# Kernel tuning notes

Measured on AMD Instinct MI355X. Metric: run time of the kernel, lower is better.

The kernel has to match this reference:

```python
import jax, jax.numpy as jnp
import numpy as np

LN2 = 0.6931471805599453

def ssp(t):
    # PhysNet shifted softplus
    return jax.nn.softplus(t) - LN2

N, F, K, E, NRES = 50000, 128, 64, 800000, 3

def setup_inputs() -> dict:
    key = jax.random.key(0)
    ks = jax.random.split(key, 16)
    d = {}
    d['x'] = jax.random.normal(ks[0], (N, F), dtype=jnp.float32)
    d['edge_index'] = jax.random.randint(ks[1], (2, E), 0, N, dtype=jnp.int64)
    d['edge_attr'] = jax.random.uniform(ks[2], (E, K), dtype=jnp.float32)
    s = 1.0 / np.sqrt(F)
    d['W_same'] = jax.random.normal(ks[3], (F, F), dtype=jnp.float32) * s
    d['b_same'] = jnp.zeros((F,), jnp.float32)
    d['W_diff'] = jax.random.normal(ks[4], (F, F), dtype=jnp.float32) * s
    d['b_diff'] = jnp.zeros((F,), jnp.float32)
    # G initialized to zero in the original; use small random so gradients flow
    d['W_G'] = jax.random.normal(ks[5], (F, K), dtype=jnp.float32) * 0.01
    d['res_W1'] = jax.random.normal(ks[6], (NRES, F, F), dtype=jnp.float32) * s
    d['res_b1'] = jnp.zeros((NRES, F), jnp.float32)
    d['res_W2'] = jax.random.normal(ks[7], (NRES, F, F), dtype=jnp.float32) * s
    d['res_b2'] = jnp.zeros((NRES, F), jnp.float32)
    d['W_last'] = jax.random.normal(ks[8], (F, F), dtype=jnp.float32) * s
    d['b_last'] = jnp.zeros((F,), jnp.float32)
    d['u'] = jnp.ones((1, F), jnp.float32)
    return d

def reference(x, edge_index, edge_attr, W_same, b_same, W_diff, b_diff, W_G,
              res_W1, res_b1, res_W2, res_b2, W_last, b_last, u):
    src, dst = edge_index[0], edge_index[1]  # flow='source_to_target': x_j = x[src], aggr at dst
    xa = ssp(x)                                           # activation(x) before propagate
    # message: act(lin_for_diff(x_j)) -- linear+act commute with gather, compute per-node
    h = ssp(xa @ W_diff.T + b_diff)                       # [N, F]
    gate = edge_attr @ W_G.T                              # [E, F]  G(edge_attr)
    msg = h[src] * gate                                   # [E, F]
    aggr = jax.ops.segment_sum(msg, dst, num_segments=x.shape[0])  # add-aggregate
    # update: act(lin_for_same(x)) + aggr_out
    msged_x = ssp(xa @ W_same.T + b_same) + aggr          # [N, F]
    # residual interaction layers: t + lin2(act(lin1(act(t))))
    t = msged_x
    for i in range(res_W1.shape[0]):
        h1 = ssp(ssp(t) @ res_W1[i].T + res_b1[i])
        t = t + (h1 @ res_W2[i].T + res_b2[i])
    v = ssp(t) @ W_last.T + b_last
    return (v + x * u, msged_x)
```

## Files before the change

kernel.cpp:

```cpp
#include <hip/hip_runtime.h>
#include <hip/hip_bf16.h>

#define LN2F 0.69314718055994530942f

typedef short bf16x8 __attribute__((ext_vector_type(8)));
typedef float f32x4  __attribute__((ext_vector_type(4)));

__device__ __forceinline__ float ssp_f(float t){
  return fmaxf(t, 0.0f) + __logf(1.0f + __expf(-fabsf(t))) - LN2F;
}
__device__ __forceinline__ unsigned short f2bf_u(float f){
  __hip_bfloat16 b = __float2bfloat16(f);
  return *reinterpret_cast<unsigned short*>(&b);
}
__device__ __forceinline__ float bf2f(unsigned short u){
  __hip_bfloat16 b = *reinterpret_cast<__hip_bfloat16*>(&u);
  return __bfloat162float(b);
}

__device__ __forceinline__ int load_idx(const void* ei, int is32, size_t pos){
  return is32 ? ((const int*)ei)[pos] : (int)(((const long long*)ei)[pos]);
}

struct WPtrs { const float* w[16]; };

__global__ __launch_bounds__(256) void setup_prep_kernel(
    const unsigned* __restrict__ ei, int* __restrict__ flag,
    int* __restrict__ count, int N, int nzb,
    WPtrs p, int nw, unsigned short* __restrict__ wfrag,
    const float* __restrict__ WG, unsigned short* __restrict__ wgfrag){
  const int m = blockIdx.x;
  if (m < nzb){
    int i = m * 256 + threadIdx.x;
    if (i < N) count[i] = 0;
    if (m == 0){
      __shared__ int cnt;
      if (threadIdx.x == 0) cnt = 0;
      __syncthreads();
      int nz = 0;
      for (int k = threadIdx.x; k < 1024; k += 256)
        nz += (ei[2*k + 1] != 0u) ? 1 : 0;
      atomicAdd(&cnt, nz);
      __syncthreads();
      if (threadIdx.x == 0) *flag = (cnt > 64) ? 1 : 0;
    }
  } else if (m < nzb + nw){
    const int w = m - nzb;
    const float* __restrict__ W = p.w[w];
    unsigned short* __restrict__ out = wfrag + (size_t)w * 16384;
    for (int q = threadIdx.x; q < 16384; q += 256){
      int i = q & 7, lane = (q >> 3) & 63, kt = (q >> 9) & 3, ct = q >> 11;
      int row = ct*16 + (lane & 15);
      int k   = kt*32 + (lane >> 4)*8 + i;
      out[q] = f2bf_u(W[row*128 + k]);
    }
  } else {
    const int b = m - nzb - nw;
    for (int qq = threadIdx.x; qq < 2048; qq += 256){
      int q = b*2048 + qq;
      int i = q & 7, lane = (q >> 3) & 63, kt = (q >> 9) & 1, nt = q >> 10;
      int f = nt*16 + (lane & 15);
      int k = kt*32 + (lane >> 4)*8 + i;
      wgfrag[q] = f2bf_u(WG[(size_t)f*64 + k]);
    }
  }
}

__global__ void hist_kernel(const void* __restrict__ ei, const int* __restrict__ flag,
                            int* __restrict__ count, int E){
  const int is32 = *flag;
  for (long long e = (long long)blockIdx.x * 256 + threadIdx.x; e < E;
       e += (long long)gridDim.x * 256){
    int d = load_idx(ei, is32, (size_t)((long long)E + e));
    atomicAdd(&count[d], 1);
  }
}

__global__ __launch_bounds__(256) void scan1_kernel(const int* __restrict__ count,
                                                    int* __restrict__ bsum, int N){
  __shared__ int red[256];
  const int t = threadIdx.x;
  int i0 = blockIdx.x * 2048 + t * 8;
  int s = 0;
  #pragma unroll
  for (int r = 0; r < 8; ++r){ int i = i0 + r; s += (i < N) ? count[i] : 0; }
  red[t] = s;
  __syncthreads();
  for (int off = 128; off > 0; off >>= 1){
    if (t < off) red[t] += red[t + off];
    __syncthreads();
  }
  if (t == 0) bsum[blockIdx.x] = red[0];
}

__global__ void scan2_kernel(int* __restrict__ bsum, int* __restrict__ offs, int nb, int N){
  if (threadIdx.x == 0 && blockIdx.x == 0){
    int run = 0;
    for (int b = 0; b < nb; ++b){ int v = bsum[b]; bsum[b] = run; run += v; }
    offs[N] = run;
  }
}

__global__ __launch_bounds__(256) void scan3_kernel(const int* __restrict__ count,
                                                    const int* __restrict__ bsum,
                                                    int* __restrict__ offs,
                                                    int* __restrict__ cur, int N){
  __shared__ int red[256];
  const int t = threadIdx.x;
  int i0 = blockIdx.x * 2048 + t * 8;
  int v[8];
  int s = 0;
  #pragma unroll
  for (int r = 0; r < 8; ++r){ int i = i0 + r; v[r] = (i < N) ? count[i] : 0; s += v[r]; }
  red[t] = s;
  __syncthreads();
  #pragma unroll
  for (int off = 1; off < 256; off <<= 1){
    int tv = (t >= off) ? red[t - off] : 0;
    __syncthreads();
    red[t] += tv;
    __syncthreads();
  }
  int run = red[t] - s + bsum[blockIdx.x];
  #pragma unroll
  for (int r = 0; r < 8; ++r){
    int i = i0 + r;
    if (i < N){ offs[i] = run; cur[i] = run; }
    run += v[r];
  }
}

__global__ void fill_kernel(const void* __restrict__ ei, const int* __restrict__ flag,
                            int* __restrict__ cur, int2* __restrict__ se, int E){
  const int is32 = *flag;
  for (long long e = (long long)blockIdx.x * 256 + threadIdx.x; e < E;
       e += (long long)gridDim.x * 256){
    int s = load_idx(ei, is32, (size_t)e);
    int d = load_idx(ei, is32, (size_t)((long long)E + e));
    int slot = atomicAdd(&cur[d], 1);
    se[slot] = make_int2((int)e, s);
  }
}

__device__ __forceinline__ void mfma_gemm128s(const unsigned short* __restrict__ A_s,
                                              const unsigned short* __restrict__ Bf,
                                              int rbase, int lane, f32x4 acc[8]){
  #pragma unroll
  for (int ct = 0; ct < 8; ++ct) acc[ct] = (f32x4){0.f, 0.f, 0.f, 0.f};
  const int r  = rbase + (lane & 15);
  const int kg = lane >> 4;
  const int sw = (r & 7) << 3;
  #pragma unroll
  for (int kt = 0; kt < 4; ++kt){
    bf16x8 a = *(const bf16x8*)&A_s[r*128 + ((kt*32 + kg*8) ^ sw)];
    #pragma unroll
    for (int ct = 0; ct < 8; ++ct){
      bf16x8 b = *(const bf16x8*)&Bf[(size_t)((ct*4 + kt)*64 + lane)*8];
      acc[ct] = __builtin_amdgcn_mfma_f32_16x16x32_bf16(a, b, acc[ct], 0, 0, 0);
    }
  }
}

__device__ __forceinline__ void stage_bf512(unsigned short* __restrict__ Bf,
                                            const unsigned short* __restrict__ src, int t){
  #pragma unroll
  for (int it = 0; it < 4; ++it){
    int off = (it*512 + t) * 8;
    *(uint4*)&Bf[off] = *(const uint4*)&src[off];
  }
}

__global__ __launch_bounds__(512) void node_dual_kernel(
    const float* __restrict__ x, const unsigned short* __restrict__ wfrag,
    const float* __restrict__ bsame, const float* __restrict__ bdiff,
    unsigned short* __restrict__ hbf, float* __restrict__ msged, int N){
  __shared__ __align__(16) unsigned short A_s[128*128];
  __shared__ __align__(16) unsigned short Bf[16384];
  const int t = threadIdx.x, wv = t >> 6, lane = t & 63;
  const int kg = lane >> 4, c = lane & 15;
  const int row0 = blockIdx.x * 128;
  for (int q = t; q < 2048; q += 512){
    int row = q >> 4, c0 = (q & 15) * 8;
    float4 va = make_float4(0.f,0.f,0.f,0.f), vb = va;
    if (row0 + row < N){
      va = *(const float4*)&x[(size_t)(row0 + row)*128 + c0];
      vb = *(const float4*)&x[(size_t)(row0 + row)*128 + c0 + 4];
    }
    uint4 w;
    w.x = f2bf_u(ssp_f(va.x)) | ((unsigned)f2bf_u(ssp_f(va.y)) << 16);
    w.y = f2bf_u(ssp_f(va.z)) | ((unsigned)f2bf_u(ssp_f(va.w)) << 16);
    w.z = f2bf_u(ssp_f(vb.x)) | ((unsigned)f2bf_u(ssp_f(vb.y)) << 16);
    w.w = f2bf_u(ssp_f(vb.z)) | ((unsigned)f2bf_u(ssp_f(vb.w)) << 16);
    *(uint4*)&A_s[row*128 + (c0 ^ ((row & 7) << 3))] = w;
  }
  stage_bf512(Bf, wfrag, t);
  __syncthreads();
  f32x4 acc[8];
  mfma_gemm128s(A_s, Bf, wv*16, lane, acc);
  #pragma unroll
  for (int ct = 0; ct < 8; ++ct){
    int col = ct*16 + c;
    float bv = bsame[col];
    #pragma unroll
    for (int q = 0; q < 4; ++q){
      int gr = row0 + wv*16 + kg*4 + q;
      if (gr < N) msged[(size_t)gr*128 + col] = ssp_f(acc[ct][q] + bv);
    }
  }
  __syncthreads();
  stage_bf512(Bf, wfrag + 16384, t);
  __syncthreads();
  mfma_gemm128s(A_s, Bf, wv*16, lane, acc);
  #pragma unroll
  for (int ct = 0; ct < 8; ++ct){
    int col = ct*16 + c;
    float bv = bdiff[col];
    #pragma unroll
    for (int q = 0; q < 4; ++q){
      int gr = row0 + wv*16 + kg*4 + q;
      if (gr < N) hbf[(size_t)gr*128 + col] = f2bf_u(ssp_f(acc[ct][q] + bv));
    }
  }
}

__global__ __launch_bounds__(256) void edge_mfma_kernel(
    const float* __restrict__ ea, const unsigned short* __restrict__ wgfrag,
    const unsigned short* __restrict__ h, const int2* __restrict__ se,
    const int* __restrict__ offs, float* __restrict__ msged, int N, int E, int KW){
  __shared__ float gate_s[4][16][132];
  __shared__ unsigned short h_s[4][16][136];
  const int t = threadIdx.x, wv = t >> 6, lane = t & 63;
  const int kg = lane >> 4, c = lane & 15;
  const int widx = blockIdx.x * 4 + wv;
  if (widx >= KW) return;
  long long tt0 = (long long)widx * E / KW;
  long long tt1 = (long long)(widx + 1) * E / KW;
  int lo = 0, hi = N;
  while (lo < hi){ int mid = (lo + hi) >> 1; if ((long long)offs[mid] < tt0) lo = mid + 1; else hi = mid; }
  const int d_lo = lo;
  hi = N;
  while (lo < hi){ int mid = (lo + hi) >> 1; if ((long long)offs[mid] < tt1) lo = mid + 1; else hi = mid; }
  const int d_hi = lo;
  if (d_lo >= d_hi) return;
  const int s_beg = offs[d_lo], s_end = offs[d_hi];
  if (s_beg >= s_end) return;

  bf16x8 aw[8][2];
  #pragma unroll
  for (int nt = 0; nt < 8; ++nt)
    #pragma unroll
    for (int kt = 0; kt < 2; ++kt)
      aw[nt][kt] = *(const bf16x8*)&wgfrag[(size_t)(((nt*2+kt)*64)+lane)*8];

  int d_cur = d_lo;
  int no0 = offs[d_cur + 1];
  while (no0 == s_beg && d_cur + 1 < d_hi){ ++d_cur; no0 = offs[d_cur + 1]; }
  int no1 = (d_cur + 2 <= d_hi) ? offs[d_cur + 2] : 0x7FFFFFFF;

  float sum0 = 0.f, sum1 = 0.f;
  int p = s_beg;
  int nb = min(16, s_end - p);
  int2 s2 = se[p + min(c, nb - 1)];
  while (p < s_end){
    const int pn = p + 16;
    int2 s2n = s2;
    if (pn < s_end){
      int nbn = min(16, s_end - pn);
      s2n = se[pn + min(c, nbn - 1)];
    }
    const float* __restrict__ ra = &ea[(size_t)s2.x * 64 + kg*8];
    float4 e00 = *(const float4*)&ra[0];
    float4 e01 = *(const float4*)&ra[4];
    float4 e10 = *(const float4*)&ra[32];
    float4 e11 = *(const float4*)&ra[36];

    uint4 hreg[4];
    #pragma unroll
    for (int it = 0; it < 4; ++it){
      int j = it*64 + lane;
      int row = j >> 4, seg = j & 15;
      int sr = __shfl(s2.y, row, 16);
      hreg[it] = *(const uint4*)&h[(size_t)sr*128 + seg*8];
    }
    #pragma unroll
    for (int it = 0; it < 4; ++it){
      int j = it*64 + lane;
      int row = j >> 4, seg = j & 15;
      *(uint4*)&h_s[wv][row][seg*8] = hreg[it];
    }

    bf16x8 be0, be1;
    unsigned short* b0p = (unsigned short*)&be0;
    unsigned short* b1p = (unsigned short*)&be1;
    b0p[0]=f2bf_u(e00.x); b0p[1]=f2bf_u(e00.y); b0p[2]=f2bf_u(e00.z); b0p[3]=f2bf_u(e00.w);
    b0p[4]=f2bf_u(e01.x); b0p[5]=f2bf_u(e01.y); b0p[6]=f2bf_u(e01.z); b0p[7]=f2bf_u(e01.w);
    b1p[0]=f2bf_u(e10.x); b1p[1]=f2bf_u(e10.y); b1p[2]=f2bf_u(e10.z); b1p[3]=f2bf_u(e10.w);
    b1p[4]=f2bf_u(e11.x); b1p[5]=f2bf_u(e11.y); b1p[6]=f2bf_u(e11.z); b1p[7]=f2bf_u(e11.w);

    #pragma unroll
    for (int nt = 0; nt < 8; ++nt){
      f32x4 acc = (f32x4){0.f,0.f,0.f,0.f};
      acc = __builtin_amdgcn_mfma_f32_16x16x32_bf16(aw[nt][0], be0, acc, 0, 0, 0);
      acc = __builtin_amdgcn_mfma_f32_16x16x32_bf16(aw[nt][1], be1, acc, 0, 0, 0);
      *(f32x4*)&gate_s[wv][c][nt*16 + kg*4] = acc;
    }

    asm volatile("s_waitcnt lgkmcnt(0)" ::: "memory");

    const int nbc = min(16, s_end - p);
    #pragma unroll
    for (int i = 0; i < 16; ++i){
      if (i < nbc){
        float g0 = gate_s[wv][i][lane];
        float g1 = gate_s[wv][i][lane + 64];
        float h0 = bf2f(h_s[wv][i][lane]);
        float h1 = bf2f(h_s[wv][i][lane + 64]);
        sum0 = __builtin_fmaf(g0, h0, sum0);
        sum1 = __builtin_fmaf(g1, h1, sum1);
        if (p + i + 1 == no0){
          float* mp = &msged[(size_t)d_cur*128 + lane];
          mp[0]  += sum0;
          mp[64] += sum1;
          sum0 = 0.f; sum1 = 0.f;
          do {
            ++d_cur;
            no0 = no1;
            no1 = (d_cur + 2 <= d_hi) ? offs[d_cur + 2] : 0x7FFFFFFF;
          } while (no0 == p + i + 1);
        }
      }
    }
    p = pn; s2 = s2n;
  }
}

__global__ __launch_bounds__(512) void tail_kernel(
    const float* __restrict__ msged, const float* __restrict__ x, const float* __restrict__ u,
    const unsigned short* __restrict__ wfrag,
    const float* __restrict__ rb1, const float* __restrict__ rb2,
    const float* __restrict__ blast, float* __restrict__ out0, int N, int NRES){
  __shared__ __align__(16) unsigned short A_s[128*128];
  __shared__ __align__(16) unsigned short Bf[16384];
  const int t = threadIdx.x, wv = t >> 6, lane = t & 63;
  const int kg = lane >> 4, c = lane & 15;
  const int row0 = blockIdx.x * 128;

  float treg[8][4];
  #pragma unroll
  for (int ct = 0; ct < 8; ++ct)
    #pragma unroll
    for (int q = 0; q < 4; ++q){
      int gr = row0 + wv*16 + kg*4 + q;
      treg[ct][q] = (gr < N) ? msged[(size_t)gr*128 + ct*16 + c] : 0.f;
    }

  f32x4 acc[8];
  for (int l = 0; l < NRES; ++l){
    __syncthreads();
    #pragma unroll
    for (int ct = 0; ct < 8; ++ct)
      #pragma unroll
      for (int q = 0; q < 4; ++q){
        int row = wv*16 + kg*4 + q, col = ct*16 + c;
        A_s[row*128 + (col ^ ((row & 7) << 3))] = f2bf_u(ssp_f(treg[ct][q]));
      }
    stage_bf512(Bf, wfrag + (size_t)(2 + 2*l)*16384, t);
    __syncthreads();
    mfma_gemm128s(A_s, Bf, wv*16, lane, acc);
    __syncthreads();
    #pragma unroll
    for (int ct = 0; ct < 8; ++ct){
      float bv = rb1[l*128 + ct*16 + c];
      #pragma unroll
      for (int q = 0; q < 4; ++q){
        int row = wv*16 + kg*4 + q, col = ct*16 + c;
        A_s[row*128 + (col ^ ((row & 7) << 3))] = f2bf_u(ssp_f(acc[ct][q] + bv));
      }
    }
    stage_bf512(Bf, wfrag + (size_t)(3 + 2*l)*16384, t);
    __syncthreads();
    mfma_gemm128s(A_s, Bf, wv*16, lane, acc);
    #pragma unroll
    for (int ct = 0; ct < 8; ++ct){
      float bv = rb2[l*128 + ct*16 + c];
      #pragma unroll
      for (int q = 0; q < 4; ++q) treg[ct][q] += acc[ct][q] + bv;
    }
  }
  __syncthreads();
  #pragma unroll
  for (int ct = 0; ct < 8; ++ct)
    #pragma unroll
    for (int q = 0; q < 4; ++q){
      int row = wv*16 + kg*4 + q, col = ct*16 + c;
      A_s[row*128 + (col ^ ((row & 7) << 3))] = f2bf_u(ssp_f(treg[ct][q]));
    }
  stage_bf512(Bf, wfrag + (size_t)(2 + 2*NRES)*16384, t);
  __syncthreads();
  mfma_gemm128s(A_s, Bf, wv*16, lane, acc);
  #pragma unroll
  for (int ct = 0; ct < 8; ++ct){
    int col = ct*16 + c;
    float bv = blast[col];
    float uv = u[col];
    #pragma unroll
    for (int q = 0; q < 4; ++q){
      int gr = row0 + wv*16 + kg*4 + q;
      if (gr < N){
        size_t idx = (size_t)gr*128 + col;
        out0[idx] = acc[ct][q] + bv + x[idx]*uv;
      }
    }
  }
}

extern "C" void kernel_launch(void* const* d_in, const int* in_sizes, int n_in,
                              void* d_out, int out_size, void* d_ws, size_t ws_size,
                              hipStream_t stream){
  const float* x     = (const float*)d_in[0];
  const void*  ei    = d_in[1];
  const float* ea    = (const float*)d_in[2];
  const float* Wsame = (const float*)d_in[3];
  const float* bsame = (const float*)d_in[4];
  const float* Wdiff = (const float*)d_in[5];
  const float* bdiff = (const float*)d_in[6];
  const float* WG    = (const float*)d_in[7];
  const float* rW1   = (const float*)d_in[8];
  const float* rb1   = (const float*)d_in[9];
  const float* rW2   = (const float*)d_in[10];
  const float* rb2   = (const float*)d_in[11];
  const float* Wlast = (const float*)d_in[12];
  const float* blast = (const float*)d_in[13];
  const float* u     = (const float*)d_in[14];

  const int N    = in_sizes[0] / 128;
  const int E    = in_sizes[1] / 2;
  int NRES = in_sizes[8] / (128*128);
  if (NRES > 6) NRES = 6;

  float* out0  = (float*)d_out;
  float* msged = (float*)d_out + (size_t)N * 128;

  auto align256 = [](size_t v){ return (v + 255) & ~(size_t)255; };
  const size_t o_h      = 256;
  const size_t o_count  = align256(o_h      + (size_t)N * 128 * 2);
  const size_t o_off    = align256(o_count  + (size_t)N * 4);
  const size_t o_cur    = align256(o_off    + (size_t)(N + 1) * 4);
  const size_t o_se     = align256(o_cur    + (size_t)N * 4);
  const size_t o_bsum   = align256(o_se     + (size_t)E * 8);
  const size_t o_wfrag  = align256(o_bsum   + (size_t)4096 * 4);
  const size_t o_wgfrag = align256(o_wfrag  + (size_t)16 * 16384 * 2);

  int*   flag = (int*)d_ws;
  unsigned short* hbf = (unsigned short*)((char*)d_ws + o_h);
  int* count  = (int*)((char*)d_ws + o_count);
  int* offs   = (int*)((char*)d_ws + o_off);
  int* cur    = (int*)((char*)d_ws + o_cur);
  int2* se    = (int2*)((char*)d_ws + o_se);
  int* bsum   = (int*)((char*)d_ws + o_bsum);
  unsigned short* wfrag  = (unsigned short*)((char*)d_ws + o_wfrag);
  unsigned short* wgfrag = (unsigned short*)((char*)d_ws + o_wgfrag);
  (void)ws_size;

  const int nw = 3 + 2*NRES;
  WPtrs wp;
  wp.w[0] = Wsame;
  wp.w[1] = Wdiff;
  for (int l = 0; l < NRES; ++l){
    wp.w[2 + 2*l] = rW1 + (size_t)l*16384;
    wp.w[3 + 2*l] = rW2 + (size_t)l*16384;
  }
  wp.w[2 + 2*NRES] = Wlast;
  for (int i = nw; i < 16; ++i) wp.w[i] = Wlast;

  const int nb_node = (N + 127) / 128;
  const int nzb     = (N + 255) / 256;
  const int nbk     = (N + 2047) / 2048;
  const int nb_edge = 2048;
  const int KW = nb_edge * 4;

  setup_prep_kernel<<<nzb + nw + 4, 256, 0, stream>>>((const unsigned*)ei, flag, count, N,
                                                      nzb, wp, nw, wfrag, WG, wgfrag);
  node_dual_kernel<<<nb_node, 512, 0, stream>>>(x, wfrag, bsame, bdiff, hbf, msged, N);

  hist_kernel<<<1024, 256, 0, stream>>>(ei, flag, count, E);
  scan1_kernel<<<nbk, 256, 0, stream>>>(count, bsum, N);
  scan2_kernel<<<1, 64, 0, stream>>>(bsum, offs, nbk, N);
  scan3_kernel<<<nbk, 256, 0, stream>>>(count, bsum, offs, cur, N);
  fill_kernel<<<1024, 256, 0, stream>>>(ei, flag, cur, se, E);

  edge_mfma_kernel<<<nb_edge, 256, 0, stream>>>(ea, wgfrag, hbf, se, offs, msged, N, E, KW);

  tail_kernel<<<nb_node, 512, 0, stream>>>(msged, x, u, wfrag, rb1, rb2, blast,
                                           out0, N, NRES);
}
```

Before: 360.7 us.

## Software-pipeline edge gathers through shared memory and fold scan2 into scan3

The edge kernel now prefetches the next 16-edge chunk of edge_attr rows and h rows into registers while the current chunk's MFMA gate and accumulation run. It writes them to shared memory at the end of the iteration, and edge_attr rows are now loaded coalesced and staged through a new ea_s buffer. Separately, the single-thread scan2 kernel is removed: each scan3 block sums the preceding block totals itself and the last block writes offs[N]. This is meant to hide gather latency and cut one kernel launch, at the cost of more shared memory, more registers and a redundant serial prefix loop per block.

```diff
diff --git a/kernel.cpp b/kernel.cpp
--- a/kernel.cpp
+++ b/kernel.cpp
@@ -93,20 +93,14 @@
   if (t == 0) bsum[blockIdx.x] = red[0];
 }
 
-__global__ void scan2_kernel(int* __restrict__ bsum, int* __restrict__ offs, int nb, int N){
-  if (threadIdx.x == 0 && blockIdx.x == 0){
-    int run = 0;
-    for (int b = 0; b < nb; ++b){ int v = bsum[b]; bsum[b] = run; run += v; }
-    offs[N] = run;
-  }
-}
-
 __global__ __launch_bounds__(256) void scan3_kernel(const int* __restrict__ count,
                                                     const int* __restrict__ bsum,
                                                     int* __restrict__ offs,
-                                                    int* __restrict__ cur, int N){
+                                                    int* __restrict__ cur, int N, int nbk){
   __shared__ int red[256];
   const int t = threadIdx.x;
+  int base = 0;
+  for (int b = 0; b < blockIdx.x; ++b) base += bsum[b];
   int i0 = blockIdx.x * 2048 + t * 8;
   int v[8];
   int s = 0;
@@ -121,13 +115,14 @@
     red[t] += tv;
     __syncthreads();
   }
-  int run = red[t] - s + bsum[blockIdx.x];
+  int run = red[t] - s + base;
   #pragma unroll
   for (int r = 0; r < 8; ++r){
     int i = i0 + r;
     if (i < N){ offs[i] = run; cur[i] = run; }
     run += v[r];
   }
+  if (blockIdx.x == nbk - 1 && t == 255) offs[N] = run;
 }
 
 __global__ void fill_kernel(const void* __restrict__ ei, const int* __restrict__ flag,
@@ -229,8 +224,10 @@
     const int* __restrict__ offs, float* __restrict__ msged, int N, int E, int KW){
   __shared__ float gate_s[4][16][132];
   __shared__ unsigned short h_s[4][16][136];
+  __shared__ float ea_s[4][16][68];
   const int t = threadIdx.x, wv = t >> 6, lane = t & 63;
   const int kg = lane >> 4, c = lane & 15;
+  const int srow = lane >> 4, seg = lane & 15;
   const int widx = blockIdx.x * 4 + wv;
   if (widx >= KW) return;
   long long tt0 = (long long)widx * E / KW;
@@ -261,42 +258,62 @@
   int p = s_beg;
   int nb = min(16, s_end - p);
   int2 s2 = se[p + min(c, nb - 1)];
+  {
+    uint4 er[4], hr[4];
+    #pragma unroll
+    for (int it = 0; it < 4; ++it){
+      int row = it*4 + srow;
+      int e  = __shfl(s2.x, row, 16);
+      int sr = __shfl(s2.y, row, 16);
+      er[it] = *(const uint4*)&ea[(size_t)e*64 + seg*4];
+      hr[it] = *(const uint4*)&h[(size_t)sr*128 + seg*8];
+    }
+    #pragma unroll
+    for (int it = 0; it < 4; ++it){
+      int row = it*4 + srow;
+      *(uint4*)&ea_s[wv][row][seg*4] = er[it];
+      *(uint4*)&h_s[wv][row][seg*8] = hr[it];
+    }
+  }
+  int2 s2n = s2;
+  if (p + 16 < s_end){
+    int nbn = min(16, s_end - (p + 16));
+    s2n = se[p + 16 + min(c, nbn - 1)];
+  }
+
   while (p < s_end){
     const int pn = p + 16;
-    int2 s2n = s2;
-    if (pn < s_end){
-      int nbn = min(16, s_end - pn);
-      s2n = se[pn + min(c, nbn - 1)];
-    }
-    const float* __restrict__ ra = &ea[(size_t)s2.x * 64 + kg*8];
-    float4 e00 = *(const float4*)&ra[0];
-    float4 e01 = *(const float4*)&ra[4];
-    float4 e10 = *(const float4*)&ra[32];
-    float4 e11 = *(const float4*)&ra[36];
-
-    uint4 hreg[4];
-    #pragma unroll
-    for (int it = 0; it < 4; ++it){
-      int j = it*64 + lane;
-      int row = j >> 4, seg = j & 15;
-      int sr = __shfl(s2.y, row, 16);
-      hreg[it] = *(const uint4*)&h[(size_t)sr*128 + seg*8];
-    }
-    #pragma unroll
-    for (int it = 0; it < 4; ++it){
-      int j = it*64 + lane;
-      int row = j >> 4, seg = j & 15;
-      *(uint4*)&h_s[wv][row][seg*8] = hreg[it];
+    const bool have_next = pn < s_end;
+
+    float4 f00 = *(const float4*)&ea_s[wv][c][kg*8];
+    float4 f01 = *(const float4*)&ea_s[wv][c][kg*8 + 4];
+    float4 f10 = *(const float4*)&ea_s[wv][c][32 + kg*8];
+    float4 f11 = *(const float4*)&ea_s[wv][c][32 + kg*8 + 4];
+
+    uint4 er[4], hr[4];
+    if (have_next){
+      #pragma unroll
+      for (int it = 0; it < 4; ++it){
+        int row = it*4 + srow;
+        int e  = __shfl(s2n.x, row, 16);
+        int sr = __shfl(s2n.y, row, 16);
+        er[it] = *(const uint4*)&ea[(size_t)e*64 + seg*4];
+        hr[it] = *(const uint4*)&h[(size_t)sr*128 + seg*8];
+      }
+    }
+    int2 s2nn = s2n;
+    if (pn + 16 < s_end){
+      int nb2 = min(16, s_end - (pn + 16));
+      s2nn = se[pn + 16 + min(c, nb2 - 1)];
     }
 
     bf16x8 be0, be1;
     unsigned short* b0p = (unsigned short*)&be0;
     unsigned short* b1p = (unsigned short*)&be1;
-    b0p[0]=f2bf_u(e00.x); b0p[1]=f2bf_u(e00.y); b0p[2]=f2bf_u(e00.z); b0p[3]=f2bf_u(e00.w);
-    b0p[4]=f2bf_u(e01.x); b0p[5]=f2bf_u(e01.y); b0p[6]=f2bf_u(e01.z); b0p[7]=f2bf_u(e01.w);
-    b1p[0]=f2bf_u(e10.x); b1p[1]=f2bf_u(e10.y); b1p[2]=f2bf_u(e10.z); b1p[3]=f2bf_u(e10.w);
-    b1p[4]=f2bf_u(e11.x); b1p[5]=f2bf_u(e11.y); b1p[6]=f2bf_u(e11.z); b1p[7]=f2bf_u(e11.w);
-
+    b0p[0]=f2bf_u(f00.x); b0p[1]=f2bf_u(f00.y); b0p[2]=f2bf_u(f00.z); b0p[3]=f2bf_u(f00.w);
+    b0p[4]=f2bf_u(f01.x); b0p[5]=f2bf_u(f01.y); b0p[6]=f2bf_u(f01.z); b0p[7]=f2bf_u(f01.w);
+    b1p[0]=f2bf_u(f10.x); b1p[1]=f2bf_u(f10.y); b1p[2]=f2bf_u(f10.z); b1p[3]=f2bf_u(f10.w);
+    b1p[4]=f2bf_u(f11.x); b1p[5]=f2bf_u(f11.y); b1p[6]=f2bf_u(f11.z); b1p[7]=f2bf_u(f11.w);
     #pragma unroll
     for (int nt = 0; nt < 8; ++nt){
       f32x4 acc = (f32x4){0.f,0.f,0.f,0.f};
@@ -330,7 +347,16 @@
         }
       }
     }
-    p = pn; s2 = s2n;
+
+    if (have_next){
+      #pragma unroll
+      for (int it = 0; it < 4; ++it){
+        int row = it*4 + srow;
+        *(uint4*)&ea_s[wv][row][seg*4] = er[it];
+        *(uint4*)&h_s[wv][row][seg*8] = hr[it];
+      }
+    }
+    p = pn; s2 = s2n; s2n = s2nn;
   }
 }
 
@@ -485,8 +511,7 @@
 
   hist_kernel<<<1024, 256, 0, stream>>>(ei, flag, count, E);
   scan1_kernel<<<nbk, 256, 0, stream>>>(count, bsum, N);
-  scan2_kernel<<<1, 64, 0, stream>>>(bsum, offs, nbk, N);
-  scan3_kernel<<<nbk, 256, 0, stream>>>(count, bsum, offs, cur, N);
+  scan3_kernel<<<nbk, 256, 0, stream>>>(count, bsum, offs, cur, N, nbk);
   fill_kernel<<<1024, 256, 0, stream>>>(ei, flag, cur, se, E);
 
   edge_mfma_kernel<<<nb_edge, 256, 0, stream>>>(ea, wgfrag, hbf, se, offs, msged, N, E, KW);
```

New measurement: 449.3 us. 1.25x slower.

## Double-buffer weights in tail kernel over 256 rows and fold scan2 into scan3

Applied to the files above, without the earlier changes.

The tail kernel now handles 256 rows per block in two 128-row slices that share each staged weight matrix. The next weight matrix is prefetched into registers and written to a second LDS buffer while the current GEMMs run, leaving one barrier per GEMM stage. The separate single-thread scan2 launch is removed; each scan3 block sums the preceding block totals itself and the last block writes the final offset. In exchange LDS use doubles (64KB A plus 64KB B), which lowers occupancy, and the register count rises because of the two-slice state and the prefetch registers.

```diff
diff --git a/kernel.cpp b/kernel.cpp
--- a/kernel.cpp
+++ b/kernel.cpp
@@ -93,20 +93,14 @@
   if (t == 0) bsum[blockIdx.x] = red[0];
 }
 
-__global__ void scan2_kernel(int* __restrict__ bsum, int* __restrict__ offs, int nb, int N){
-  if (threadIdx.x == 0 && blockIdx.x == 0){
-    int run = 0;
-    for (int b = 0; b < nb; ++b){ int v = bsum[b]; bsum[b] = run; run += v; }
-    offs[N] = run;
-  }
-}
-
 __global__ __launch_bounds__(256) void scan3_kernel(const int* __restrict__ count,
                                                     const int* __restrict__ bsum,
                                                     int* __restrict__ offs,
-                                                    int* __restrict__ cur, int N){
+                                                    int* __restrict__ cur, int N, int nbk){
   __shared__ int red[256];
   const int t = threadIdx.x;
+  int base = 0;
+  for (int b = 0; b < blockIdx.x; ++b) base += bsum[b];
   int i0 = blockIdx.x * 2048 + t * 8;
   int v[8];
   int s = 0;
@@ -121,13 +115,14 @@
     red[t] += tv;
     __syncthreads();
   }
-  int run = red[t] - s + bsum[blockIdx.x];
+  int run = red[t] - s + base;
   #pragma unroll
   for (int r = 0; r < 8; ++r){
     int i = i0 + r;
     if (i < N){ offs[i] = run; cur[i] = run; }
     run += v[r];
   }
+  if (blockIdx.x == nbk - 1 && t == 255) offs[N] = run;
 }
 
 __global__ void fill_kernel(const void* __restrict__ ei, const int* __restrict__ flag,
@@ -339,78 +334,87 @@
     const unsigned short* __restrict__ wfrag,
     const float* __restrict__ rb1, const float* __restrict__ rb2,
     const float* __restrict__ blast, float* __restrict__ out0, int N, int NRES){
-  __shared__ __align__(16) unsigned short A_s[128*128];
-  __shared__ __align__(16) unsigned short Bf[16384];
+  __shared__ __align__(16) unsigned short A_s[256*128];
+  __shared__ __align__(16) unsigned short Bf[2][16384];
   const int t = threadIdx.x, wv = t >> 6, lane = t & 63;
   const int kg = lane >> 4, c = lane & 15;
-  const int row0 = blockIdx.x * 128;
-
-  float treg[8][4];
-  #pragma unroll
-  for (int ct = 0; ct < 8; ++ct)
-    #pragma unroll
-    for (int q = 0; q < 4; ++q){
-      int gr = row0 + wv*16 + kg*4 + q;
-      treg[ct][q] = (gr < N) ? msged[(size_t)gr*128 + ct*16 + c] : 0.f;
-    }
-
-  f32x4 acc[8];
-  for (int l = 0; l < NRES; ++l){
-    __syncthreads();
+  const int row0 = blockIdx.x * 256;
+
+  float treg[2][8][4];
+  #pragma unroll
+  for (int sl = 0; sl < 2; ++sl)
     #pragma unroll
     for (int ct = 0; ct < 8; ++ct)
       #pragma unroll
       for (int q = 0; q < 4; ++q){
-        int row = wv*16 + kg*4 + q, col = ct*16 + c;
-        A_s[row*128 + (col ^ ((row & 7) << 3))] = f2bf_u(ssp_f(treg[ct][q]));
+        int gr = row0 + sl*128 + wv*16 + kg*4 + q;
+        float v = (gr < N) ? msged[(size_t)gr*128 + ct*16 + c] : 0.f;
+        treg[sl][ct][q] = v;
+        int row = sl*128 + wv*16 + kg*4 + q, col = ct*16 + c;
+        A_s[row*128 + (col ^ ((row & 7) << 3))] = f2bf_u(ssp_f(v));
       }
-    stage_bf512(Bf, wfrag + (size_t)(2 + 2*l)*16384, t);
+
+  stage_bf512(Bf[0], wfrag + (size_t)2*16384, t);
+  __syncthreads();
+
+  const int NG = 2*NRES + 1;
+  int cur = 0;
+  for (int g = 0; g < NG; ++g){
+    const bool more = (g + 1 < NG);
+    uint4 wr[4];
+    if (more){
+      const unsigned short* __restrict__ src = wfrag + (size_t)(3 + g)*16384;
+      #pragma unroll
+      for (int it = 0; it < 4; ++it) wr[it] = *(const uint4*)&src[(it*512 + t)*8];
+    }
+    const int l = g >> 1;
+    #pragma unroll
+    for (int sl = 0; sl < 2; ++sl){
+      f32x4 acc[8];
+      mfma_gemm128s(A_s + sl*16384, Bf[cur], wv*16, lane, acc);
+      if (g == NG - 1){
+        #pragma unroll
+        for (int ct = 0; ct < 8; ++ct){
+          int col = ct*16 + c;
+          float bv = blast[col], uv = u[col];
+          #pragma unroll
+          for (int q = 0; q < 4; ++q){
+            int gr = row0 + sl*128 + wv*16 + kg*4 + q;
+            if (gr < N){
+              size_t idx = (size_t)gr*128 + col;
+              out0[idx] = acc[ct][q] + bv + x[idx]*uv;
+            }
+          }
+        }
+      } else if ((g & 1) == 0){
+        #pragma unroll
+        for (int ct = 0; ct < 8; ++ct){
+          float bv = rb1[l*128 + ct*16 + c];
+          #pragma unroll
+          for (int q = 0; q < 4; ++q){
+            int row = sl*128 + wv*16 + kg*4 + q, col = ct*16 + c;
+            A_s[row*128 + (col ^ ((row & 7) << 3))] = f2bf_u(ssp_f(acc[ct][q] + bv));
+          }
+        }
+      } else {
+        #pragma unroll
+        for (int ct = 0; ct < 8; ++ct){
+          float bv = rb2[l*128 + ct*16 + c];
+          #pragma unroll
+          for (int q = 0; q < 4; ++q){
+            treg[sl][ct][q] += acc[ct][q] + bv;
+            int row = sl*128 + wv*16 + kg*4 + q, col = ct*16 + c;
+            A_s[row*128 + (col ^ ((row & 7) << 3))] = f2bf_u(ssp_f(treg[sl][ct][q]));
+          }
+        }
+      }
+    }
+    if (more){
+      #pragma unroll
+      for (int it = 0; it < 4; ++it) *(uint4*)&Bf[cur ^ 1][(it*512 + t)*8] = wr[it];
+    }
     __syncthreads();
-    mfma_gemm128s(A_s, Bf, wv*16, lane, acc);
-    __syncthreads();
-    #pragma unroll
-    for (int ct = 0; ct < 8; ++ct){
-      float bv = rb1[l*128 + ct*16 + c];
-      #pragma unroll
-      for (int q = 0; q < 4; ++q){
-        int row = wv*16 + kg*4 + q, col = ct*16 + c;
-        A_s[row*128 + (col ^ ((row & 7) << 3))] = f2bf_u(ssp_f(acc[ct][q] + bv));
-      }
-    }
-    stage_bf512(Bf, wfrag + (size_t)(3 + 2*l)*16384, t);
-    __syncthreads();
-    mfma_gemm128s(A_s, Bf, wv*16, lane, acc);
-    #pragma unroll
-    for (int ct = 0; ct < 8; ++ct){
-      float bv = rb2[l*128 + ct*16 + c];
-      #pragma unroll
-      for (int q = 0; q < 4; ++q) treg[ct][q] += acc[ct][q] + bv;
-    }
-  }
-  __syncthreads();
-  #pragma unroll
-  for (int ct = 0; ct < 8; ++ct)
-    #pragma unroll
-    for (int q = 0; q < 4; ++q){
-      int row = wv*16 + kg*4 + q, col = ct*16 + c;
-      A_s[row*128 + (col ^ ((row & 7) << 3))] = f2bf_u(ssp_f(treg[ct][q]));
-    }
-  stage_bf512(Bf, wfrag + (size_t)(2 + 2*NRES)*16384, t);
-  __syncthreads();
-  mfma_gemm128s(A_s, Bf, wv*16, lane, acc);
-  #pragma unroll
-  for (int ct = 0; ct < 8; ++ct){
-    int col = ct*16 + c;
-    float bv = blast[col];
-    float uv = u[col];
-    #pragma unroll
-    for (int q = 0; q < 4; ++q){
-      int gr = row0 + wv*16 + kg*4 + q;
-      if (gr < N){
-        size_t idx = (size_t)gr*128 + col;
-        out0[idx] = acc[ct][q] + bv + x[idx]*uv;
-      }
-    }
+    cur ^= 1;
   }
 }
 
@@ -473,10 +477,11 @@
   wp.w[2 + 2*NRES] = Wlast;
   for (int i = nw; i < 16; ++i) wp.w[i] = Wlast;
 
-  const int nb_node = (N + 127) / 128;
-  const int nzb     = (N + 255) / 256;
-  const int nbk     = (N + 2047) / 2048;
-  const int nb_edge = 2048;
+  const int nb_node  = (N + 127) / 128;
+  const int nb_node2 = (N + 255) / 256;
+  const int nzb      = (N + 255) / 256;
+  const int nbk      = (N + 2047) / 2048;
+  const int nb_edge  = 2048;
   const int KW = nb_edge * 4;
 
   setup_prep_kernel<<<nzb + nw + 4, 256, 0, stream>>>((const unsigned*)ei, flag, count, N,
@@ -485,12 +490,11 @@
 
   hist_kernel<<<1024, 256, 0, stream>>>(ei, flag, count, E);
   scan1_kernel<<<nbk, 256, 0, stream>>>(count, bsum, N);
-  scan2_kernel<<<1, 64, 0, stream>>>(bsum, offs, nbk, N);
-  scan3_kernel<<<nbk, 256, 0, stream>>>(count, bsum, offs, cur, N);
+  scan3_kernel<<<nbk, 256, 0, stream>>>(count, bsum, offs, cur, N, nbk);
   fill_kernel<<<1024, 256, 0, stream>>>(ei, flag, cur, se, E);
 
   edge_mfma_kernel<<<nb_edge, 256, 0, stream>>>(ea, wgfrag, hbf, se, offs, msged, N, E, KW);
 
-  tail_kernel<<<nb_node, 512, 0, stream>>>(msged, x, u, wfrag, rb1, rb2, blast,
-                                           out0, N, NRES);
-}
+  tail_kernel<<<nb_node2, 512, 0, stream>>>(msged, x, u, wfrag, rb1, rb2, blast,
+                                            out0, N, NRES);
+}
```

Measured after the change: 483.5 us. 34.0% more time.
